# Optimization experiments

Measured on AMD Instinct MI355X. Metric: run time of the kernel, lower is better.

The kernel has to match this reference:

```python
import jax, jax.numpy as jnp
from jax import lax
import numpy as np

# constants from module construction: segmentation_loss3D(alpha=1.0, percentile=95)
ALPHA_T = 1.0          # tversky alpha
BETA_T = 2.0 - ALPHA_T # tversky beta
EPS = 1e-5
HD_ALPHA = 2.0         # HausdorffDTLoss default alpha
BIG = 1e9              # stand-in for +inf in the min-plus distance transform


def _dt1d(f, axis):
    """Exact 1D squared Euclidean distance transform along `axis`:
    d[i] = min_j f[j] + (i - j)^2, computed as a min-plus scan over j."""
    n = f.shape[axis]
    fT = jnp.moveaxis(f, axis, 0)                      # (n, ...)
    idx = jnp.arange(n, dtype=f.dtype)
    d0 = jnp.full(fT.shape[1:] + (n,), BIG, f.dtype)   # (..., n)

    def step(d, xs):
        fj, j = xs
        return jnp.minimum(d, fj[..., None] + (idx - j) ** 2), None

    d, _ = lax.scan(step, d0, (fT, idx))
    return jnp.moveaxis(d, -1, axis)


def _edt(mask):
    """Euclidean distance to the nearest False voxel (matches scipy edt),
    over all axes except the two leading (stack, batch) axes."""
    f = jnp.where(mask, jnp.float32(BIG), jnp.float32(0.0))
    for ax in range(2, mask.ndim):
        f = _dt1d(f, ax)
    return jnp.sqrt(f)


def _distance_fields(pred, target_oh):
    # scipy loop runs edt over the full (C, X, Y, Z) array per batch element
    imgs = jnp.stack([pred, target_oh])           # (2, B, C, X, Y, Z)
    fg = imgs > 0.5
    masks = jnp.concatenate([fg, ~fg], axis=0)    # (4, B, C, X, Y, Z)
    dist = _edt(masks)
    field = dist[:2] + dist[2:]                   # fg_dist + bg_dist
    has_fg = jnp.any(fg, axis=(2, 3, 4, 5))       # (2, B) -- torch.no_grad guard
    field = jnp.where(has_fg[:, :, None, None, None, None], field, 0.0)
    field = lax.stop_gradient(field)
    return field[0], field[1]


def setup_inputs() -> dict:
    key = jax.random.key(0)
    k1, k2 = jax.random.split(key)
    B, C, X, Y, Z = 2, 8, 64, 64, 64
    inputs = jax.random.normal(k1, (B, C, X, Y, Z), dtype=jnp.float32)
    targets = jax.random.randint(k2, (B, X, Y, Z), 0, C, dtype=jnp.int32)
    return {"inputs": inputs, "targets": targets}


def reference(inputs, targets):
    C = inputs.shape[1]
    t_oh = jax.nn.one_hot(targets, C, axis=1, dtype=inputs.dtype)  # (B,C,X,Y,Z)

    # --- tversky (dice) loss ---
    probs = jax.nn.softmax(inputs, axis=1)
    red = tuple(range(2, inputs.ndim))
    tps = jnp.sum(probs * t_oh, red)
    fps = jnp.sum(probs * (1.0 - t_oh), red) * ALPHA_T
    fns = jnp.sum((1.0 - probs) * t_oh, red) * BETA_T
    score = 2.0 * tps / (2.0 * tps + fps + fns + EPS)   # (B, C)
    dice = 1.0 - jnp.mean(score, axis=0)[1:].mean()

    # --- cross entropy (mean over all voxels) ---
    logp = jax.nn.log_softmax(inputs, axis=1)
    ce = -jnp.mean(jnp.take_along_axis(logp, targets[:, None].astype(jnp.int32), axis=1))

    # --- Hausdorff distance-transform loss ---
    pred_dt, target_dt = _distance_fields(inputs, t_oh)
    pred_error = (inputs - t_oh) ** 2
    distance = pred_dt ** HD_ALPHA + target_dt ** HD_ALPHA
    hd = jnp.mean(pred_error * distance)

    return dice + ce + hd
```

## Files before the change

### kernel.cpp

```cpp
#include <hip/hip_runtime.h>

#define NVOX (64 * 64 * 64)
#define FMU (16 * NVOX)
#define FM (16 * NVOX)


__device__ __forceinline__ float unpack_val(unsigned short p) {
    int v = p & 0x7fff;
    return (v == 32767) ? 1e9f : (float)v;
}


__global__ __launch_bounds__(256) void k_zy2(const float* __restrict__ in,
                                             const int* __restrict__ tg,
                                             unsigned short* __restrict__ f) {
    __shared__ float tile[64 * 65];
    unsigned short* tile16 = (unsigned short*)tile;
    int blk = blockIdx.x;
    int src = blk >> 10;
    int s = blk & 1023;
    int b = s >> 9, c = (s >> 6) & 7, x = s & 63;
    int w = threadIdx.x >> 6;
    int lane = threadIdx.x & 63;

    const float* pin = in + (b * 8 + c) * NVOX + x * 4096;
    const int* ptg = tg + b * NVOX + x * 4096;

    float dB[16];
#pragma unroll
    for (int k = 0; k < 16; ++k) {
        int y = k * 4 + w;
        bool member;
        if (src == 0) member = pin[y * 64 + lane] > 0.5f;
        else          member = ptg[y * 64 + lane] == c;
        unsigned long long mkA = __ballot(!member);
        unsigned long long mkB = ~mkA;
        unsigned long long sfA = mkA << (63 - lane), sbA = mkA >> lane;
        int dfA = sfA ? __builtin_clzll(sfA) : 64;
        int dbA = sbA ? __builtin_ctzll(sbA) : 64;
        int da = dfA < dbA ? dfA : dbA;
        unsigned long long sfB = mkB << (63 - lane), sbB = mkB >> lane;
        int dfB = sfB ? __builtin_clzll(sfB) : 64;
        int dbB = sbB ? __builtin_ctzll(sbB) : 64;
        int db = dfB < dbB ? dfB : dbB;
        tile[y * 65 + lane] = (da > 63) ? 1e9f : (float)(da * da);
        dB[k] = (db > 63) ? 1e9f : (float)(db * db);
    }
    __syncthreads();

    float rA[16];
#pragma unroll
    for (int k = 0; k < 16; ++k) {
        int z = k * 4 + w;
        float d = tile[lane * 65 + z];
        int q = 1;
        for (int dd = 1; dd <= 63 && (float)q < d; ++dd) {
            int jl = lane - dd, jr = lane + dd;
            float cl = (jl >= 0) ? tile[jl * 65 + z] : 1e9f;
            float cr = (jr < 64) ? tile[jr * 65 + z] : 1e9f;
            d = fminf(d, fminf(cl, cr) + (float)q);
            q += 2 * dd + 1;
        }
        rA[k] = fminf(d, 1e9f);
    }
    __syncthreads();

#pragma unroll
    for (int k = 0; k < 16; ++k) tile[(k * 4 + w) * 65 + lane] = dB[k];
    __syncthreads();

    float rB[16];
#pragma unroll
    for (int k = 0; k < 16; ++k) {
        int z = k * 4 + w;
        float d = tile[lane * 65 + z];
        int q = 1;
        for (int dd = 1; dd <= 63 && (float)q < d; ++dd) {
            int jl = lane - dd, jr = lane + dd;
            float cl = (jl >= 0) ? tile[jl * 65 + z] : 1e9f;
            float cr = (jr < 64) ? tile[jr * 65 + z] : 1e9f;
            d = fminf(d, fminf(cl, cr) + (float)q);
            q += 2 * dd + 1;
        }
        rB[k] = fminf(d, 1e9f);
    }
    __syncthreads();

#pragma unroll
    for (int k = 0; k < 16; ++k) {
        int z = k * 4 + w;
        float tot = rA[k] + rB[k];
        int vi = (int)fminf(tot, 32767.f);
        tile16[lane * 65 + z] =
            (unsigned short)(((rB[k] == 0.f) ? 0x8000 : 0) | vi);
    }
    __syncthreads();

    unsigned short* out = f + (size_t)src * FMU + (b * 8 + c) * NVOX + x * 4096;
#pragma unroll
    for (int k = 0; k < 16; ++k) {
        int y = k * 4 + w;
        out[y * 64 + lane] = tile16[y * 65 + lane];
    }
}

__global__ __launch_bounds__(256) void k_xdt(unsigned short* __restrict__ f) {
    __shared__ float tile[64 * 65];
    unsigned short* tile16 = (unsigned short*)tile;
    int blk = blockIdx.x;
    int src = blk >> 10;
    int s = blk & 1023;
    int b = s >> 9, c = (s >> 6) & 7, y = s & 63;
    int w = threadIdx.x >> 6;
    int lane = threadIdx.x & 63;

    unsigned short* base = f + (size_t)src * FMU + (b * 8 + c) * NVOX + y * 64;

    float dB0[16];
#pragma unroll
    for (int k = 0; k < 16; ++k) {
        int x = k * 4 + w;
        unsigned short p = base[x * 4096 + lane];
        float fv = unpack_val(p);
        bool member = (p & 0x8000) != 0;
        tile[x * 65 + lane] = member ? fv : 0.f;
        dB0[k] = member ? 0.f : fv;
    }
    __syncthreads();

    float rA[16];
#pragma unroll
    for (int k = 0; k < 16; ++k) {
        int z = k * 4 + w;
        float d = tile[lane * 65 + z];
        int q = 1;
        for (int dd = 1; dd <= 63 && (float)q < d; ++dd) {
            int jl = lane - dd, jr = lane + dd;
            float cl = (jl >= 0) ? tile[jl * 65 + z] : 1e9f;
            float cr = (jr < 64) ? tile[jr * 65 + z] : 1e9f;
            d = fminf(d, fminf(cl, cr) + (float)q);
            q += 2 * dd + 1;
        }
        rA[k] = fminf(d, 1e9f);
    }
    __syncthreads();

#pragma unroll
    for (int k = 0; k < 16; ++k) tile[(k * 4 + w) * 65 + lane] = dB0[k];
    __syncthreads();

    float rB[16];
#pragma unroll
    for (int k = 0; k < 16; ++k) {
        int z = k * 4 + w;
        float d = tile[lane * 65 + z];
        int q = 1;
        for (int dd = 1; dd <= 63 && (float)q < d; ++dd) {
            int jl = lane - dd, jr = lane + dd;
            float cl = (jl >= 0) ? tile[jl * 65 + z] : 1e9f;
            float cr = (jr < 64) ? tile[jr * 65 + z] : 1e9f;
            d = fminf(d, fminf(cl, cr) + (float)q);
            q += 2 * dd + 1;
        }
        rB[k] = fminf(d, 1e9f);
    }
    __syncthreads();

#pragma unroll
    for (int k = 0; k < 16; ++k) {
        int z = k * 4 + w;
        float tot = rA[k] + rB[k];
        int vi = (int)fminf(tot, 32767.f);
        tile16[lane * 65 + z] =
            (unsigned short)(((rB[k] == 0.f) ? 0x8000 : 0) | vi);
    }
    __syncthreads();

#pragma unroll
    for (int k = 0; k < 16; ++k) {
        int x = k * 4 + w;
        base[x * 4096 + lane] = tile16[x * 65 + lane];
    }
}

__global__ __launch_bounds__(256) void k_chds(const float* __restrict__ in,
                                              const int* __restrict__ tg,
                                              const unsigned short* __restrict__ f,
                                              float* __restrict__ statP,
                                              double* __restrict__ predS,
                                              double* __restrict__ tgtS) {
    __shared__ float part[4][27];
    __shared__ int af;
    if (threadIdx.x == 0) af = 0;
    __syncthreads();

    int blk = blockIdx.x;
    int v = blk * 256 + threadIdx.x;
    int b = v >> 18;
    int r = v & (NVOX - 1);
    int t = tg[v];
    int lane = threadIdx.x & 63;
    int wid = threadIdx.x >> 6;

    float xs[8], ex[8];
#pragma unroll
    for (int c = 0; c < 8; ++c) xs[c] = in[(b * 8 + c) * NVOX + r];
    float mx = xs[0];
#pragma unroll
    for (int c = 1; c < 8; ++c) mx = fmaxf(mx, xs[c]);
    float se = 0.f;
#pragma unroll
    for (int c = 0; c < 8; ++c) { ex[c] = expf(xs[c] - mx); se += ex[c]; }
    float inv = 1.f / se;
    float lse = mx + logf(se);
    float xt = xs[0];
#pragma unroll
    for (int c = 1; c < 8; ++c) xt = (t == c) ? xs[c] : xt;

    bool anyP = false;
    float red[17];
    float cnt[8];
#pragma unroll
    for (int c = 0; c < 8; ++c) {
        float p = ex[c] * inv;
        red[c] = p;
        red[8 + c] = (t == c) ? p : 0.f;
        cnt[c] = (float)__popcll(__ballot(t == c));
        anyP = anyP || (xs[c] > 0.5f);
    }
    red[16] = lse - xt;

#pragma unroll
    for (int k = 0; k < 17; ++k) {
        float s = red[k];
        s += __shfl_down(s, 32);
        s += __shfl_down(s, 16);
        s += __shfl_down(s, 8);
        s += __shfl_down(s, 4);
        s += __shfl_down(s, 2);
        s += __shfl_down(s, 1);
        red[k] = s;
    }
    bool wav = __any(anyP);
    if (lane == 0) {
#pragma unroll
        for (int k = 0; k < 8; ++k) part[wid][k] = red[k];
#pragma unroll
        for (int k = 0; k < 8; ++k) part[wid][8 + k] = red[8 + k];
#pragma unroll
        for (int k = 0; k < 8; ++k) part[wid][16 + k] = cnt[k];
        part[wid][24] = red[16];
        if (wav) atomicOr(&af, 1);
    }

    float e2[8];
#pragma unroll
    for (int c = 0; c < 8; ++c) {
        float e = xs[c] - ((t == c) ? 1.f : 0.f);
        e2[c] = e * e;
    }
    float accP = 0.f, accT = 0.f;
#pragma unroll
    for (int src = 0; src < 2; ++src) {
        float fmA[8], fmB[8];
#pragma unroll
        for (int c = 0; c < 8; ++c) {
            unsigned short p = f[(size_t)src * FMU + (b * 8 + c) * NVOX + r];
            float fv = unpack_val(p);
            bool member = (p & 0x8000) != 0;
            fmA[c] = member ? fv : 0.f;
            fmB[c] = member ? 0.f : fv;
        }
        float am = 0.f;
#pragma unroll
        for (int i = 0; i < 8; ++i) {
            float da = 1e9f, db = 1e9f;
#pragma unroll
            for (int j = 0; j < 8; ++j) {
                float q = (float)((i - j) * (i - j));
                da = fminf(da, fmA[j] + q);
                db = fminf(db, fmB[j] + q);
            }
            am += e2[i] * (da + db);
        }
        if (src) accT += am; else accP += am;
    }
#pragma unroll
    for (int off = 32; off >= 1; off >>= 1) {
        accP += __shfl_down(accP, off);
        accT += __shfl_down(accT, off);
    }
    if (lane == 0) { part[wid][25] = accP; part[wid][26] = accT; }
    __syncthreads();

    int j = blk & 1023;
    if (threadIdx.x < 25)
        statP[(b * 26 + threadIdx.x) * 1024 + j] =
            part[0][threadIdx.x] + part[1][threadIdx.x] +
            part[2][threadIdx.x] + part[3][threadIdx.x];
    if (threadIdx.x == 25)
        statP[(b * 26 + 25) * 1024 + j] = af ? 1.f : 0.f;
    if (threadIdx.x == 26)
        predS[blk] = (double)part[0][25] + (double)part[1][25] +
                     (double)part[2][25] + (double)part[3][25];
    if (threadIdx.x == 27)
        tgtS[blk] = (double)part[0][26] + (double)part[1][26] +
                    (double)part[2][26] + (double)part[3][26];
}

__global__ __launch_bounds__(256) void k_final3(const float* __restrict__ statP,
                                                const double* __restrict__ predS,
                                                const double* __restrict__ tgtS,
                                                float* __restrict__ out) {
    __shared__ float rs[52];
    __shared__ double rd[4];
    int tid = threadIdx.x;
    int w = tid >> 6;
    int lane = tid & 63;

    for (int row = w; row < 52; row += 4) {
        const float* p = statP + row * 1024;
        float s = 0.f;
#pragma unroll
        for (int k = 0; k < 16; ++k) s += p[k * 64 + lane];
        s += __shfl_down(s, 32);
        s += __shfl_down(s, 16);
        s += __shfl_down(s, 8);
        s += __shfl_down(s, 4);
        s += __shfl_down(s, 2);
        s += __shfl_down(s, 1);
        if (lane == 0) rs[row] = s;
    }
    {
        const double* p = (w < 2) ? (predS + w * 1024) : (tgtS + (w - 2) * 1024);
        double s = 0.0;
#pragma unroll
        for (int k = 0; k < 16; ++k) s += p[k * 64 + lane];
        s += __shfl_down(s, 32);
        s += __shfl_down(s, 16);
        s += __shfl_down(s, 8);
        s += __shfl_down(s, 4);
        s += __shfl_down(s, 2);
        s += __shfl_down(s, 1);
        if (lane == 0) rd[w] = s;
    }
    __syncthreads();

    if (tid == 0) {
        bool fP0 = rs[0 * 26 + 25] > 0.f;
        bool fP1 = rs[1 * 26 + 25] > 0.f;
        double h = (fP0 ? rd[0] : 0.0) + (fP1 ? rd[1] : 0.0) + rd[2] + rd[3];
        float dsum = 0.f;
        for (int c = 1; c < 8; ++c) {
            float sc = 0.f;
            for (int b = 0; b < 2; ++b) {
                float S1 = rs[b * 26 + c];
                float S2 = rs[b * 26 + 8 + c];
                float Nc = rs[b * 26 + 16 + c];
                sc += 2.f * S2 / (2.f * S2 + (S1 - S2) + (Nc - S2) + 1e-5f);
            }
            dsum += sc * 0.5f;
        }
        float dice = 1.f - dsum / 7.f;
        float ce = (rs[0 * 26 + 24] + rs[1 * 26 + 24]) / 524288.f;
        out[0] = dice + ce + (float)(h / 4194304.0);
    }
}

__global__ __launch_bounds__(256, 4) void k_stats(const float* __restrict__ in,
                                                  const int* __restrict__ tg,
                                                  float* __restrict__ accF,
                                                  int* __restrict__ flags) {
    int r = blockIdx.x * 256 + threadIdx.x;
    int lane = threadIdx.x & 63;
    int wid = threadIdx.x >> 6;
    __shared__ float part[4][25];
    __shared__ int af;

    for (int b = 0; b < 2; ++b) {
        int t = tg[b * NVOX + r];
        float xs[8];
#pragma unroll
        for (int c = 0; c < 8; ++c) xs[c] = in[(b * 8 + c) * NVOX + r];
        float mx = xs[0];
#pragma unroll
        for (int c = 1; c < 8; ++c) mx = fmaxf(mx, xs[c]);
        float ex[8];
        float se = 0.f;
#pragma unroll
        for (int c = 0; c < 8; ++c) { ex[c] = expf(xs[c] - mx); se += ex[c]; }
        float inv = 1.f / se;
        float lse = mx + logf(se);
        float xt = xs[0];
#pragma unroll
        for (int c = 1; c < 8; ++c) xt = (t == c) ? xs[c] : xt;
        bool anyP = false;
        float red[25];
#pragma unroll
        for (int c = 0; c < 8; ++c) {
            float p = ex[c] * inv;
            red[c] = p;
            red[8 + c] = (t == c) ? p : 0.f;
            red[16 + c] = (t == c) ? 1.f : 0.f;
            anyP = anyP || (xs[c] > 0.5f);
        }
        red[24] = lse - xt;
#pragma unroll
        for (int k = 0; k < 25; ++k) {
            float s = red[k];
            s += __shfl_down(s, 32);
            s += __shfl_down(s, 16);
            s += __shfl_down(s, 8);
            s += __shfl_down(s, 4);
            s += __shfl_down(s, 2);
            s += __shfl_down(s, 1);
            red[k] = s;
        }
        if (threadIdx.x == 0) af = 0;
        __syncthreads();
        bool wav = __any(anyP);
        if (lane == 0) {
#pragma unroll
            for (int k = 0; k < 25; ++k) part[wid][k] = red[k];
            if (wav) atomicOr(&af, 1);
        }
        __syncthreads();
        if (threadIdx.x < 25) {
            float s = part[0][threadIdx.x] + part[1][threadIdx.x] +
                      part[2][threadIdx.x] + part[3][threadIdx.x];
            atomicAdd(&accF[b * 25 + threadIdx.x], s);
        }
        if (threadIdx.x == 0 && af) atomicOr(&flags[b], 1);
        __syncthreads();
    }
}

template <int M0>
__global__ __launch_bounds__(64) void k_mask_zy(const float* __restrict__ in,
                                                const int* __restrict__ tg,
                                                float* __restrict__ f) {
    __shared__ float tile[64 * 65];
    int blk = blockIdx.x;
    int m = M0 + (blk >> 10);
    int s = blk & 1023;
    int b = s >> 9, c = (s >> 6) & 7, x = s & 63;
    int tid = threadIdx.x;

    if ((m & 1) == 0) {
        const float* src = in + (b * 8 + c) * NVOX + x * 4096;
#pragma unroll 8
        for (int k = 0; k < 64; ++k) {
            bool fg = src[k * 64 + tid] > 0.5f;
            bool hot = (m < 2) ? fg : !fg;
            tile[k * 65 + tid] = hot ? 1e9f : 0.f;
        }
    } else {
        const int* src = tg + b * NVOX + x * 4096;
#pragma unroll 8
        for (int k = 0; k < 64; ++k) {
            bool fg = (src[k * 64 + tid] == c);
            bool hot = (m < 2) ? fg : !fg;
            tile[k * 65 + tid] = hot ? 1e9f : 0.f;
        }
    }
    __syncthreads();
    {
        float* row = &tile[tid * 65];
        float g = 1000.f;
#pragma unroll 8
        for (int z = 0; z < 64; ++z) {
            float v = row[z];
            g = (v == 0.f) ? 0.f : g + 1.f;
            row[z] = g;
        }
        g = 1000.f;
#pragma unroll 8
        for (int z = 63; z >= 0; --z) {
            float gf = row[z];
            g = (gf == 0.f) ? 0.f : g + 1.f;
            float d = fminf(gf, g);
            row[z] = (d > 63.f) ? 1e9f : d * d;
        }
    }
    __syncthreads();
    float* out = f + (size_t)(blk >> 10) * FM + (b * 8 + c) * NVOX + x * 4096;
    for (int i = 0; i < 64; ++i) {
        float d0 = tile[i * 65 + tid];
        float d = d0;
        int Ri = (int)sqrtf(d0) + 1;
        Ri = (Ri > 63) ? 63 : Ri;
        for (int dd = 1; dd <= Ri; ++dd) {
            float q = (float)(dd * dd);
            int jl = i - dd, jr = i + dd;
            float cl = (jl >= 0) ? tile[jl * 65 + tid] : 1e9f;
            float cr = (jr < 64) ? tile[jr * 65 + tid] : 1e9f;
            d = fminf(d, fminf(cl, cr) + q);
        }
        out[i * 64 + tid] = fminf(d, 1e9f);
    }
}

template <int M0>
__global__ __launch_bounds__(128, 4) void k_dtx(float* __restrict__ f) {
    __shared__ float wl[128 * 65];
    int blk = blockIdx.x;
    int mi = blk >> 9;
    int s = blk & 511;
    int plane = s >> 5;
    int y0 = (s & 31) * 2;
    int tid = threadIdx.x;
    float* fb = f + (size_t)mi * FM + plane * NVOX + y0 * 64;

#pragma unroll 8
    for (int j = 0; j < 64; ++j) wl[tid * 65 + j] = fb[j * 4096 + tid];

    float* row = &wl[tid * 65];
    for (int i = 0; i < 64; ++i) {
        float d0 = row[i];
        float d = d0;
        int Ri = (int)sqrtf(d0) + 1;
        Ri = (Ri > 63) ? 63 : Ri;
        for (int dd = 1; dd <= Ri; ++dd) {
            float q = (float)(dd * dd);
            int jl = i - dd, jr = i + dd;
            float cl = (jl >= 0) ? row[jl] : 1e9f;
            float cr = (jr < 64) ? row[jr] : 1e9f;
            d = fminf(d, fminf(cl, cr) + q);
        }
        fb[i * 4096 + tid] = fminf(d, 1e9f);
    }
}

template <int M0, int NM>
__global__ __launch_bounds__(256, 4) void k_cdt_hd(const float* __restrict__ in,
                                                   const int* __restrict__ tg,
                                                   const float* __restrict__ f,
                                                   const int* __restrict__ flags,
                                                   double* __restrict__ hd) {
    int v = blockIdx.x * 256 + threadIdx.x;
    int b = v >> 18;
    int r = v & (NVOX - 1);
    int t = tg[v];

    float e2[8];
#pragma unroll
    for (int c = 0; c < 8; ++c) {
        float e = in[(b * 8 + c) * NVOX + r] - ((t == c) ? 1.f : 0.f);
        e2[c] = e * e;
    }
    float acc = 0.f;
#pragma unroll
    for (int mi = 0; mi < NM; ++mi) {
        int m = M0 + mi;
        float fl = (m & 1) ? 1.f : (flags[b] ? 1.f : 0.f);
        float fm[8];
#pragma unroll
        for (int c = 0; c < 8; ++c)
            fm[c] = f[(size_t)mi * FM + (b * 8 + c) * NVOX + r];
        float am = 0.f;
#pragma unroll
        for (int i = 0; i < 8; ++i) {
            float d = 1e9f;
#pragma unroll
            for (int j = 0; j < 8; ++j)
                d = fminf(d, fm[j] + (float)((i - j) * (i - j)));
            am += e2[i] * d;
        }
        acc += fl * am;
    }
    float ssum = acc;
    ssum += __shfl_down(ssum, 32);
    ssum += __shfl_down(ssum, 16);
    ssum += __shfl_down(ssum, 8);
    ssum += __shfl_down(ssum, 4);
    ssum += __shfl_down(ssum, 2);
    ssum += __shfl_down(ssum, 1);
    __shared__ float part[4];
    int lane = threadIdx.x & 63;
    int wid = threadIdx.x >> 6;
    if (lane == 0) part[wid] = ssum;
    __syncthreads();
    if (threadIdx.x == 0)
        atomicAdd(hd, (double)(part[0] + part[1] + part[2] + part[3]));
}

__global__ void k_final(const float* __restrict__ accF,
                        const double* __restrict__ hd,
                        float* __restrict__ out) {
    float dsum = 0.f;
    for (int c = 1; c < 8; ++c) {
        float sc = 0.f;
        for (int b = 0; b < 2; ++b) {
            float S1 = accF[b * 25 + c];
            float S2 = accF[b * 25 + 8 + c];
            float Nc = accF[b * 25 + 16 + c];
            sc += 2.f * S2 / (2.f * S2 + (S1 - S2) + (Nc - S2) + 1e-5f);
        }
        dsum += sc * 0.5f;
    }
    float dice = 1.f - dsum / 7.f;
    float ce = (accF[24] + accF[25 + 24]) / 524288.f;
    float hdv = (float)(hd[0] / 4194304.0);
    out[0] = dice + ce + hdv;
}

template <int M0, int NM>
static void run_chunk(const float* in, const int* tg, float* f,
                      const int* flags, double* hd, hipStream_t stream) {
    k_mask_zy<M0><<<NM * 1024, 64, 0, stream>>>(in, tg, f);
    k_dtx<M0><<<NM * 512, 128, 0, stream>>>(f);
    k_cdt_hd<M0, NM><<<2048, 256, 0, stream>>>(in, tg, f, flags, hd);
}

extern "C" void kernel_launch(void* const* d_in, const int* in_sizes, int n_in,
                              void* d_out, int out_size, void* d_ws, size_t ws_size,
                              hipStream_t stream) {
    const float* in = (const float*)d_in[0];
    const int* tg = (const int*)d_in[1];
    float* out = (float*)d_out;

    size_t offF = (size_t)2 * FMU * 2;
    size_t need_fast = offF + 16384 + 16384 + 52 * 1024 * 4;

    if (ws_size >= need_fast) {
        unsigned short* fu = (unsigned short*)d_ws;
        double* predS = (double*)((char*)d_ws + offF);
        double* tgtS = (double*)((char*)d_ws + offF + 16384);
        float* statP = (float*)((char*)d_ws + offF + 32768);
        k_zy2<<<2048, 256, 0, stream>>>(in, tg, fu);
        k_xdt<<<2048, 256, 0, stream>>>(fu);
        k_chds<<<2048, 256, 0, stream>>>(in, tg, fu, statP, predS, tgtS);
        k_final3<<<1, 256, 0, stream>>>(statP, predS, tgtS, out);
    } else {
        float* f = (float*)d_ws;
        size_t acc_off = ((ws_size - 256) / 256) * 256;
        char* accB = (char*)d_ws + acc_off;
        double* hd = (double*)accB;
        float* accF = (float*)(accB + 8);
        int* flags = (int*)(accB + 208);
        hipMemsetAsync(accB, 0, 256, stream);
        k_stats<<<1024, 256, 0, stream>>>(in, tg, accF, flags);
        int nm_cap = (int)(acc_off / ((size_t)FM * 4));
        if (nm_cap >= 2) {
            run_chunk<0, 2>(in, tg, f, flags, hd, stream);
            run_chunk<2, 2>(in, tg, f, flags, hd, stream);
        } else if (nm_cap >= 1) {
            run_chunk<0, 1>(in, tg, f, flags, hd, stream);
            run_chunk<1, 1>(in, tg, f, flags, hd, stream);
            run_chunk<2, 1>(in, tg, f, flags, hd, stream);
            run_chunk<3, 1>(in, tg, f, flags, hd, stream);
        }
        k_final<<<1, 1, 0, stream>>>(accF, hd, out);
    }
}
```

Measured before the change: 139.8 us.

## Merge foreground and background distance transforms into one signed-value pass

Each voxel belongs to only one of the two complementary masks, so the foreground and background 1D distance transforms are computed together in one pass. The pass stores a signed tile where the sign marks membership and seeds each voxel with the ballot-derived distance to the nearest opposite voxel. This removes the second scan, a tile refill and two barriers in both the zy and x kernels, which roughly halves the LDS scan work. In exchange the inner loop does an extra multiply and select per neighbour, and correctness depends on the seeding matching the separate-pass result exactly.

```diff
diff --git a/kernel.cpp b/kernel.cpp
--- a/kernel.cpp
+++ b/kernel.cpp
@@ -26,7 +26,6 @@
     const float* pin = in + (b * 8 + c) * NVOX + x * 4096;
     const int* ptg = tg + b * NVOX + x * 4096;
 
-    float dB[16];
 #pragma unroll
     for (int k = 0; k < 16; ++k) {
         int y = k * 4 + w;
@@ -34,65 +33,57 @@
         if (src == 0) member = pin[y * 64 + lane] > 0.5f;
         else          member = ptg[y * 64 + lane] == c;
         unsigned long long mkA = __ballot(!member);
-        unsigned long long mkB = ~mkA;
-        unsigned long long sfA = mkA << (63 - lane), sbA = mkA >> lane;
-        int dfA = sfA ? __builtin_clzll(sfA) : 64;
-        int dbA = sbA ? __builtin_ctzll(sbA) : 64;
-        int da = dfA < dbA ? dfA : dbA;
-        unsigned long long sfB = mkB << (63 - lane), sbB = mkB >> lane;
-        int dfB = sfB ? __builtin_clzll(sfB) : 64;
-        int dbB = sbB ? __builtin_ctzll(sbB) : 64;
-        int db = dfB < dbB ? dfB : dbB;
-        tile[y * 65 + lane] = (da > 63) ? 1e9f : (float)(da * da);
-        dB[k] = (db > 63) ? 1e9f : (float)(db * db);
+        unsigned long long sm = member ? mkA : ~mkA;
+        unsigned long long sf = sm << (63 - lane), sb = sm >> lane;
+        int df = sf ? __builtin_clzll(sf) : 64;
+        int db = sb ? __builtin_ctzll(sb) : 64;
+        int dz = df < db ? df : db;
+        float pv = (dz > 63) ? 1e9f : (float)(dz * dz);
+        tile[y * 65 + lane] = member ? -pv : pv;
     }
     __syncthreads();
 
     float rA[16];
+    bool mreg[16];
 #pragma unroll
     for (int k = 0; k < 16; ++k) {
         int z = k * 4 + w;
-        float d = tile[lane * 65 + z];
+        float sv = tile[lane * 65 + z];
+        bool m = sv < 0.f;
+        float pv = fabsf(sv);
+        float msign = m ? -1.f : 1.f;
+        unsigned long long mw = __ballot(m);
+        unsigned long long xm = m ? ~mw : mw;
+        unsigned long long sf = xm << (63 - lane), sb = xm >> lane;
+        int df = sf ? __builtin_clzll(sf) : 64;
+        int db = sb ? __builtin_ctzll(sb) : 64;
+        int dopp = df < db ? df : db;
+        float d = fminf(pv, (dopp > 63) ? 1e9f : (float)(dopp * dopp));
         int q = 1;
         for (int dd = 1; dd <= 63 && (float)q < d; ++dd) {
             int jl = lane - dd, jr = lane + dd;
-            float cl = (jl >= 0) ? tile[jl * 65 + z] : 1e9f;
-            float cr = (jr < 64) ? tile[jr * 65 + z] : 1e9f;
+            float cl = 1e9f, cr = 1e9f;
+            if (jl >= 0) {
+                float t = tile[jl * 65 + z] * msign;
+                cl = (t > 0.f) ? t : 1e9f;
+            }
+            if (jr < 64) {
+                float t = tile[jr * 65 + z] * msign;
+                cr = (t > 0.f) ? t : 1e9f;
+            }
             d = fminf(d, fminf(cl, cr) + (float)q);
             q += 2 * dd + 1;
         }
         rA[k] = fminf(d, 1e9f);
-    }
-    __syncthreads();
-
-#pragma unroll
-    for (int k = 0; k < 16; ++k) tile[(k * 4 + w) * 65 + lane] = dB[k];
-    __syncthreads();
-
-    float rB[16];
+        mreg[k] = m;
+    }
+    __syncthreads();
+
 #pragma unroll
     for (int k = 0; k < 16; ++k) {
         int z = k * 4 + w;
-        float d = tile[lane * 65 + z];
-        int q = 1;
-        for (int dd = 1; dd <= 63 && (float)q < d; ++dd) {
-            int jl = lane - dd, jr = lane + dd;
-            float cl = (jl >= 0) ? tile[jl * 65 + z] : 1e9f;
-            float cr = (jr < 64) ? tile[jr * 65 + z] : 1e9f;
-            d = fminf(d, fminf(cl, cr) + (float)q);
-            q += 2 * dd + 1;
-        }
-        rB[k] = fminf(d, 1e9f);
-    }
-    __syncthreads();
-
-#pragma unroll
-    for (int k = 0; k < 16; ++k) {
-        int z = k * 4 + w;
-        float tot = rA[k] + rB[k];
-        int vi = (int)fminf(tot, 32767.f);
-        tile16[lane * 65 + z] =
-            (unsigned short)(((rB[k] == 0.f) ? 0x8000 : 0) | vi);
+        int vi = (int)fminf(rA[k], 32767.f);
+        tile16[lane * 65 + z] = (unsigned short)((mreg[k] ? 0x8000 : 0) | vi);
     }
     __syncthreads();
 
@@ -116,63 +107,56 @@
 
     unsigned short* base = f + (size_t)src * FMU + (b * 8 + c) * NVOX + y * 64;
 
-    float dB0[16];
 #pragma unroll
     for (int k = 0; k < 16; ++k) {
         int x = k * 4 + w;
         unsigned short p = base[x * 4096 + lane];
-        float fv = unpack_val(p);
-        bool member = (p & 0x8000) != 0;
-        tile[x * 65 + lane] = member ? fv : 0.f;
-        dB0[k] = member ? 0.f : fv;
+        float v = unpack_val(p);
+        tile[x * 65 + lane] = (p & 0x8000) ? -v : v;
     }
     __syncthreads();
 
     float rA[16];
+    bool mreg[16];
 #pragma unroll
     for (int k = 0; k < 16; ++k) {
         int z = k * 4 + w;
-        float d = tile[lane * 65 + z];
+        float sv = tile[lane * 65 + z];
+        bool m = sv < 0.f;
+        float pv = fabsf(sv);
+        float msign = m ? -1.f : 1.f;
+        unsigned long long mw = __ballot(m);
+        unsigned long long xm = m ? ~mw : mw;
+        unsigned long long sf = xm << (63 - lane), sb = xm >> lane;
+        int df = sf ? __builtin_clzll(sf) : 64;
+        int db = sb ? __builtin_ctzll(sb) : 64;
+        int dopp = df < db ? df : db;
+        float d = fminf(pv, (dopp > 63) ? 1e9f : (float)(dopp * dopp));
         int q = 1;
         for (int dd = 1; dd <= 63 && (float)q < d; ++dd) {
             int jl = lane - dd, jr = lane + dd;
-            float cl = (jl >= 0) ? tile[jl * 65 + z] : 1e9f;
-            float cr = (jr < 64) ? tile[jr * 65 + z] : 1e9f;
+            float cl = 1e9f, cr = 1e9f;
+            if (jl >= 0) {
+                float t = tile[jl * 65 + z] * msign;
+                cl = (t > 0.f) ? t : 1e9f;
+            }
+            if (jr < 64) {
+                float t = tile[jr * 65 + z] * msign;
+                cr = (t > 0.f) ? t : 1e9f;
+            }
             d = fminf(d, fminf(cl, cr) + (float)q);
             q += 2 * dd + 1;
         }
         rA[k] = fminf(d, 1e9f);
-    }
-    __syncthreads();
-
-#pragma unroll
-    for (int k = 0; k < 16; ++k) tile[(k * 4 + w) * 65 + lane] = dB0[k];
-    __syncthreads();
-
-    float rB[16];
+        mreg[k] = m;
+    }
+    __syncthreads();
+
 #pragma unroll
     for (int k = 0; k < 16; ++k) {
         int z = k * 4 + w;
-        float d = tile[lane * 65 + z];
-        int q = 1;
-        for (int dd = 1; dd <= 63 && (float)q < d; ++dd) {
-            int jl = lane - dd, jr = lane + dd;
-            float cl = (jl >= 0) ? tile[jl * 65 + z] : 1e9f;
-            float cr = (jr < 64) ? tile[jr * 65 + z] : 1e9f;
-            d = fminf(d, fminf(cl, cr) + (float)q);
-            q += 2 * dd + 1;
-        }
-        rB[k] = fminf(d, 1e9f);
-    }
-    __syncthreads();
-
-#pragma unroll
-    for (int k = 0; k < 16; ++k) {
-        int z = k * 4 + w;
-        float tot = rA[k] + rB[k];
-        int vi = (int)fminf(tot, 32767.f);
-        tile16[lane * 65 + z] =
-            (unsigned short)(((rB[k] == 0.f) ? 0x8000 : 0) | vi);
+        int vi = (int)fminf(rA[k], 32767.f);
+        tile16[lane * 65 + z] = (unsigned short)((mreg[k] ? 0x8000 : 0) | vi);
     }
     __syncthreads();
 
```

Measured after the change: 141.3 us. No clear change (+1.1%).
